# Kernel tuning notes

Measured on AMD Instinct MI355X. Metric: run time of the kernel, lower is better.

Reference implementation:

```python
import jax, jax.numpy as jnp
import numpy as np
import math

DIM = 1024
NUM_HEADS = 16
HEAD_DIM = DIM // NUM_HEADS
MAX_SEQ_LEN = 2048


def setup_inputs() -> dict:
    key = jax.random.key(0)
    ks = jax.random.split(key, 10)
    B, S = 4, 2048
    std = 1.0 / math.sqrt(DIM)
    inp = {
        "x": jax.random.normal(ks[0], (B, S, DIM), dtype=jnp.float32),
        "key_padding_mask": jnp.zeros((B, S), dtype=jnp.bool_),
        "q_w": jax.random.uniform(ks[1], (DIM, DIM), minval=-std, maxval=std),
        "q_b": jax.random.uniform(ks[2], (DIM,), minval=-std, maxval=std),
        "k_w": jax.random.uniform(ks[3], (DIM, DIM), minval=-std, maxval=std),
        "k_b": jax.random.uniform(ks[4], (DIM,), minval=-std, maxval=std),
        "v_w": jax.random.uniform(ks[5], (DIM, DIM), minval=-std, maxval=std),
        "v_b": jax.random.uniform(ks[6], (DIM,), minval=-std, maxval=std),
        "o_w": jax.random.uniform(ks[7], (DIM, DIM), minval=-std, maxval=std),
        "o_b": jax.random.uniform(ks[8], (DIM,), minval=-std, maxval=std),
    }
    return inp


def _rope_tables(seq_len):
    # freqs over half the head dim, per the RotaryPositionalEmbedding module
    half = HEAD_DIM // 2
    freqs = 1.0 / (10000.0 ** (jnp.arange(0, HEAD_DIM, 2, dtype=jnp.float32) / HEAD_DIM))
    pos = jnp.arange(seq_len, dtype=jnp.float32)
    ang = jnp.outer(pos, freqs)  # [S, half]
    return jnp.cos(ang)[:, :half], jnp.sin(ang)[:, :half]


def _apply_rope(t, cos, sin):
    # t: [B, H, S, D]; rotate first/second halves (non-interleaved variant)
    half = HEAD_DIM // 2
    left, right = t[..., :half], t[..., half:]
    return jnp.concatenate([left * cos - right * sin,
                            left * sin + right * cos], axis=-1)


def reference(x, key_padding_mask, q_w, q_b, k_w, k_b, v_w, v_b, o_w, o_b):
    B, S, _ = x.shape
    scale = HEAD_DIM ** -0.5

    def proj(w, b):
        y = jnp.einsum('bsd,ed->bse', x, w) + b  # torch Linear: x @ W^T + b
        return y.reshape(B, S, NUM_HEADS, HEAD_DIM).transpose(0, 2, 1, 3)

    q = proj(q_w, q_b)  # [B, H, S, D]
    k = proj(k_w, k_b)
    v = proj(v_w, v_b)

    cos, sin = _rope_tables(S)  # [S, half], broadcast over B,H
    q = _apply_rope(q, cos, sin)
    k = _apply_rope(k, cos, sin)

    scores = jnp.einsum('bhqd,bhkd->bhqk', q, k) * scale
    scores = jnp.where(key_padding_mask[:, None, None, :], -1e9, scores)
    weights = jax.nn.softmax(scores, axis=-1)  # dropout p=0.0 -> identity
    out = jnp.einsum('bhqk,bhkd->bhqd', weights, v)
    out = out.transpose(0, 2, 1, 3).reshape(B, S, DIM)
    return jnp.einsum('bsd,ed->bse', out, o_w) + o_b
```

## Files before the change

### kernel.cpp

```cpp
#include <hip/hip_runtime.h>
#include <stdint.h>

#define SEQ   2048
#define BATCH 4
#define NH    16
#define HD    64
#define DIMN  1024
#define MROWS (BATCH*SEQ)

typedef __attribute__((ext_vector_type(8)))  short          bf16x8;
typedef __attribute__((ext_vector_type(8)))  unsigned short ushort8;
typedef __attribute__((ext_vector_type(4)))  float          f32x4;
typedef __attribute__((ext_vector_type(16))) float          f32x16;

static __device__ __forceinline__ unsigned short f2bf(float f) {
    unsigned int u = __builtin_bit_cast(unsigned int, f);
    u += 0x7fffu + ((u >> 16) & 1u);
    return (unsigned short)(u >> 16);
}
static __device__ __forceinline__ unsigned int pack2bf(float lo, float hi) {
    unsigned int a = __builtin_bit_cast(unsigned int, lo) + 0x8000u;
    unsigned int b = __builtin_bit_cast(unsigned int, hi) + 0x8000u;
    return __builtin_amdgcn_perm(b, a, 0x07060302u);
}
static __device__ __forceinline__ unsigned int pack2bf_trunc(float lo, float hi) {
    return __builtin_amdgcn_perm(__builtin_bit_cast(unsigned int, hi),
                                 __builtin_bit_cast(unsigned int, lo), 0x07060302u);
}

__global__ __launch_bounds__(256) void prologue_kernel(
        const float* __restrict__ x,
        const float* __restrict__ qw, const float* __restrict__ kw,
        const float* __restrict__ vw, const float* __restrict__ ow,
        unsigned short* __restrict__ xb,
        unsigned short* __restrict__ wq, unsigned short* __restrict__ wk,
        unsigned short* __restrict__ wv, unsigned short* __restrict__ wo,
        float* __restrict__ cosT, float* __restrict__ sinT,
        const unsigned char* __restrict__ mask, unsigned long long* __restrict__ m64) {
    const int bx = blockIdx.x, tid = threadIdx.x;
    if (bx < 4096 + 2048) {
        const float* s; unsigned short* d; int i;
        if (bx < 4096) { s = x; d = xb; i = bx * 2048 + tid * 8; }
        else {
            int wb = bx - 4096;
            int wsel = wb >> 9;
            s = wsel == 0 ? qw : (wsel == 1 ? kw : (wsel == 2 ? vw : ow));
            d = wsel == 0 ? wq : (wsel == 1 ? wk : (wsel == 2 ? wv : wo));
            i = (wb & 511) * 2048 + tid * 8;
        }
        float4 a = *(const float4*)(s + i);
        float4 b = *(const float4*)(s + i + 4);
        ushort8 o;
        o[0]=f2bf(a.x); o[1]=f2bf(a.y); o[2]=f2bf(a.z); o[3]=f2bf(a.w);
        o[4]=f2bf(b.x); o[5]=f2bf(b.y); o[6]=f2bf(b.z); o[7]=f2bf(b.w);
        *(ushort8*)(d + i) = o;
    } else if (bx < 6400) {
        int idx = (bx - 6144) * 256 + tid;
        int s = idx >> 5, j = idx & 31;
        float t = (float)(2 * j) / 64.0f;
        float freq = 1.0f / powf(10000.0f, t);
        float ang  = (float)s * freq;
        cosT[idx] = cosf(ang);
        sinT[idx] = sinf(ang);
    } else {
        if (tid < 128) {
            int b = tid >> 5, kt = tid & 31;
            const unsigned char* p = mask + b * SEQ + kt * 64;
            unsigned long long v = 0;
            for (int j = 0; j < 64; j++) v |= (unsigned long long)(p[j] != 0) << j;
            m64[tid] = v;
        }
    }
}

__global__ __launch_bounds__(256) void gemm_qkvt(const unsigned short* __restrict__ X,
        const unsigned short* __restrict__ Wq, const unsigned short* __restrict__ Wk,
        const unsigned short* __restrict__ Wv,
        const float* __restrict__ bq, const float* __restrict__ bk, const float* __restrict__ bv,
        unsigned short* __restrict__ Qo, unsigned short* __restrict__ Ko, unsigned short* __restrict__ Vto,
        const float* __restrict__ cosT, const float* __restrict__ sinT) {
    __shared__ __align__(16) unsigned short As0[128 * 32];
    __shared__ __align__(16) unsigned short Bs0[128 * 32];
    __shared__ __align__(16) unsigned short As1[128 * 32];
    __shared__ __align__(16) unsigned short Bs1[128 * 32];
    const int which = blockIdx.x >> 3;
    const int tid  = threadIdx.x;
    const int wid  = tid >> 6, lane = tid & 63;
    const int quad = lane >> 4, l15 = lane & 15;
    const int wm   = wid >> 1,  wn  = wid & 1;

    const unsigned short *Ag, *Bg;
    int m0, n0;
    if (which < 2) {
        m0 = blockIdx.y * 128;
        n0 = (blockIdx.x & 7) * 128;
        Ag = X;  Bg = which == 0 ? Wq : Wk;
    } else {
        m0 = (blockIdx.x & 7) * 128;
        n0 = blockIdx.y * 128;
        Ag = Wv; Bg = X;
    }

    f32x4 acc[4][4];
#pragma unroll
    for (int i = 0; i < 4; i++)
#pragma unroll
        for (int j = 0; j < 4; j++) acc[i][j] = (f32x4)0.0f;

    const int rb = wid * 32 + (lane >> 2);
    const int cb = (((lane & 3) ^ ((lane >> 3) & 3)) * 8);
    const int rq = (quad ^ ((l15 >> 1) & 3)) * 8;

#define GSTAGE(BA, BB, KK) do {                                                             \
    _Pragma("unroll")                                                                       \
    for (int i_ = 0; i_ < 2; i_++) {                                                        \
        const unsigned short* ga_ = Ag + (size_t)(m0 + rb + i_ * 16) * DIMN + (KK) + cb;    \
        __builtin_amdgcn_global_load_lds((const __attribute__((address_space(1))) void*)ga_,\
            (__attribute__((address_space(3))) void*)&BA[(wid * 32 + i_ * 16) * 32], 16, 0, 0);\
        const unsigned short* gb_ = Bg + (size_t)(n0 + rb + i_ * 16) * DIMN + (KK) + cb;    \
        __builtin_amdgcn_global_load_lds((const __attribute__((address_space(1))) void*)gb_,\
            (__attribute__((address_space(3))) void*)&BB[(wid * 32 + i_ * 16) * 32], 16, 0, 0);\
    } } while (0)

#define GCOMP(BA, BB) do {                                                                  \
    bf16x8 af_[4], bf_[4];                                                                  \
    _Pragma("unroll")                                                                       \
    for (int f_ = 0; f_ < 4; f_++) af_[f_] = *(const bf16x8*)&BA[(wm * 64 + f_ * 16 + l15) * 32 + rq]; \
    _Pragma("unroll")                                                                       \
    for (int f_ = 0; f_ < 4; f_++) bf_[f_] = *(const bf16x8*)&BB[(wn * 64 + f_ * 16 + l15) * 32 + rq]; \
    _Pragma("unroll")                                                                       \
    for (int fm_ = 0; fm_ < 4; fm_++)                                                       \
        _Pragma("unroll")                                                                   \
        for (int fn_ = 0; fn_ < 4; fn_++)                                                   \
            acc[fm_][fn_] = __builtin_amdgcn_mfma_f32_16x16x32_bf16(af_[fm_], bf_[fn_], acc[fm_][fn_], 0, 0, 0); \
    } while (0)

    GSTAGE(As0, Bs0, 0);
    for (int k0 = 0; k0 < DIMN; k0 += 64) {
        __syncthreads();
        GSTAGE(As1, Bs1, k0 + 32);
        GCOMP(As0, Bs0);
        __syncthreads();
        if (k0 + 64 < DIMN) GSTAGE(As0, Bs0, k0 + 64);
        GCOMP(As1, Bs1);
    }

    if (which < 2) {
        const float* bias   = which == 0 ? bq : bk;
        unsigned short* Out = which == 0 ? Qo : Ko;
        const float scale = which == 0 ? 0.18033688011112042f : 1.0f;
        float bv4[4];
#pragma unroll
        for (int fn = 0; fn < 4; fn++) bv4[fn] = bias[n0 + wn * 64 + fn * 16 + l15];
        const int h = (n0 >> 6) + wn;
#pragma unroll
        for (int fm = 0; fm < 4; fm++)
#pragma unroll
            for (int r = 0; r < 4; r++) {
                int mrow = m0 + wm * 64 + fm * 16 + quad * 4 + r;
                int b = mrow >> 11, s = mrow & (SEQ - 1);
                unsigned short* orow = Out + ((size_t)(b * NH + h) * SEQ + s) * HD;
                float v0 = (acc[fm][0][r] + bv4[0]) * scale;
                float v1 = (acc[fm][1][r] + bv4[1]) * scale;
                float v2 = (acc[fm][2][r] + bv4[2]) * scale;
                float v3 = (acc[fm][3][r] + bv4[3]) * scale;
                int d0 = l15, d1 = 16 + l15;
                float c0 = cosT[s * 32 + d0], s0 = sinT[s * 32 + d0];
                float c1 = cosT[s * 32 + d1], s1 = sinT[s * 32 + d1];
                orow[d0]      = f2bf(v0 * c0 - v2 * s0);
                orow[d0 + 32] = f2bf(v0 * s0 + v2 * c0);
                orow[d1]      = f2bf(v1 * c1 - v3 * s1);
                orow[d1 + 32] = f2bf(v1 * s1 + v3 * c1);
            }
    } else {
        float4 bb[4];
#pragma unroll
        for (int fm = 0; fm < 4; fm++)
            bb[fm] = *(const float4*)&bv[m0 + wm * 64 + fm * 16 + quad * 4];
        const int b     = n0 >> 11;
        const int sbase = (n0 & (SEQ - 1)) + wn * 64 + l15;
#pragma unroll
        for (int fm = 0; fm < 4; fm++)
#pragma unroll
            for (int r = 0; r < 4; r++) {
                int e = m0 + wm * 64 + fm * 16 + quad * 4 + r;
                float bval = r == 0 ? bb[fm].x : (r == 1 ? bb[fm].y : (r == 2 ? bb[fm].z : bb[fm].w));
                unsigned short* row = Vto + ((size_t)(b * NH + (e >> 6)) * HD + (e & 63)) * SEQ + sbase;
#pragma unroll
                for (int fn = 0; fn < 4; fn++)
                    row[fn * 16] = f2bf(acc[fm][fn][r] + bval);
            }
    }
#undef GSTAGE
#undef GCOMP
}

__global__ __launch_bounds__(256) void gemm_bt(const unsigned short* __restrict__ A,
                                               const unsigned short* __restrict__ W,
                                               const float* __restrict__ bias,
                                               float* __restrict__ out) {
    __shared__ __align__(16) unsigned short As0[128 * 32];
    __shared__ __align__(16) unsigned short Bs0[128 * 32];
    __shared__ __align__(16) unsigned short As1[128 * 32];
    __shared__ __align__(16) unsigned short Bs1[128 * 32];
    const int tid  = threadIdx.x;
    const int wid  = tid >> 6, lane = tid & 63;
    const int quad = lane >> 4, l15 = lane & 15;
    const int wm   = wid >> 1,  wn  = wid & 1;
    const int m0   = blockIdx.y * 128, n0 = blockIdx.x * 128;

    f32x4 acc[4][4];
#pragma unroll
    for (int i = 0; i < 4; i++)
#pragma unroll
        for (int j = 0; j < 4; j++) acc[i][j] = (f32x4)0.0f;

    const int rb = wid * 32 + (lane >> 2);
    const int cb = (((lane & 3) ^ ((lane >> 3) & 3)) * 8);
    const int rq = (quad ^ ((l15 >> 1) & 3)) * 8;

#define GSTAGE(BA, BB, KK) do {                                                             \
    _Pragma("unroll")                                                                       \
    for (int i_ = 0; i_ < 2; i_++) {                                                        \
        const unsigned short* ga_ = A + (size_t)(m0 + rb + i_ * 16) * DIMN + (KK) + cb;     \
        __builtin_amdgcn_global_load_lds((const __attribute__((address_space(1))) void*)ga_,\
            (__attribute__((address_space(3))) void*)&BA[(wid * 32 + i_ * 16) * 32], 16, 0, 0);\
        const unsigned short* gb_ = W + (size_t)(n0 + rb + i_ * 16) * DIMN + (KK) + cb;     \
        __builtin_amdgcn_global_load_lds((const __attribute__((address_space(1))) void*)gb_,\
            (__attribute__((address_space(3))) void*)&BB[(wid * 32 + i_ * 16) * 32], 16, 0, 0);\
    } } while (0)

#define GCOMP(BA, BB) do {                                                                  \
    bf16x8 af_[4], bf_[4];                                                                  \
    _Pragma("unroll")                                                                       \
    for (int f_ = 0; f_ < 4; f_++) af_[f_] = *(const bf16x8*)&BA[(wm * 64 + f_ * 16 + l15) * 32 + rq]; \
    _Pragma("unroll")                                                                       \
    for (int f_ = 0; f_ < 4; f_++) bf_[f_] = *(const bf16x8*)&BB[(wn * 64 + f_ * 16 + l15) * 32 + rq]; \
    _Pragma("unroll")                                                                       \
    for (int fm_ = 0; fm_ < 4; fm_++)                                                       \
        _Pragma("unroll")                                                                   \
        for (int fn_ = 0; fn_ < 4; fn_++)                                                   \
            acc[fm_][fn_] = __builtin_amdgcn_mfma_f32_16x16x32_bf16(af_[fm_], bf_[fn_], acc[fm_][fn_], 0, 0, 0); \
    } while (0)

    GSTAGE(As0, Bs0, 0);
    for (int k0 = 0; k0 < DIMN; k0 += 64) {
        __syncthreads();
        GSTAGE(As1, Bs1, k0 + 32);
        GCOMP(As0, Bs0);
        __syncthreads();
        if (k0 + 64 < DIMN) GSTAGE(As0, Bs0, k0 + 64);
        GCOMP(As1, Bs1);
    }

    float bv4[4];
#pragma unroll
    for (int fn = 0; fn < 4; fn++) bv4[fn] = bias[n0 + wn * 64 + fn * 16 + l15];
#pragma unroll
    for (int fm = 0; fm < 4; fm++)
#pragma unroll
        for (int r = 0; r < 4; r++) {
            int mrow = m0 + wm * 64 + fm * 16 + quad * 4 + r;
            float* orow = out + (size_t)mrow * DIMN + n0 + wn * 64;
#pragma unroll
            for (int fn = 0; fn < 4; fn++) orow[fn * 16 + l15] = acc[fm][fn][r] + bv4[fn];
        }
#undef GSTAGE
#undef GCOMP
}

__global__ __launch_bounds__(256, 4) void attn_kernel(const unsigned short* __restrict__ Q,
                                                      const unsigned short* __restrict__ K,
                                                      const unsigned short* __restrict__ Vt,
                                                      const unsigned long long* __restrict__ M64,
                                                      unsigned short* __restrict__ Ob) {
    __shared__ __align__(16) unsigned short Kls[64 * 64];
    __shared__ __align__(16) unsigned short Vls[64 * 64];

    const int tid  = threadIdx.x;
    const int wid  = tid >> 6, lane = tid & 63;
    const int hi   = lane >> 5, l31 = lane & 31, l7 = lane & 7;
    const int bid = blockIdx.x;
    const int bh  = (bid & 7) * 8 + (bid >> 7);
    const int qt  = (bid >> 3) & 15;
    const int b = bh >> 4, h = bh & 15;
    const int q0 = qt * 128;

    bf16x8 qB[4];
    {
        const unsigned short* qrow = Q + ((size_t)bh * SEQ + q0 + wid * 32 + l31) * HD + hi * 8;
#pragma unroll
        for (int ks = 0; ks < 4; ks++)
            qB[ks] = __builtin_bit_cast(bf16x8, *(const uint4*)(qrow + ks * 16));
    }

    f32x16 Oa[2];
    Oa[0] = (f32x16)0.0f;
    Oa[1] = (f32x16)0.0f;
    float ls = 0.0f;

    const unsigned long long* Mrow = M64 + b * (SEQ / 64);

    const int srow = lane >> 3;
    const int sgr  = ((lane & 7) ^ ((lane >> 3) & 7)) * 8;
    const unsigned short* Kg = K  + (size_t)bh * SEQ * HD;
    const unsigned short* Vg = Vt + (size_t)bh * HD * SEQ;
    const unsigned short* Kb0 = Kg + (size_t)(wid * 16 + srow) * HD + sgr;
    const unsigned short* Vb0 = Vg + (size_t)(wid * 16 + srow) * SEQ + sgr;

    for (int kt = 0; kt < SEQ / 64; kt++) {
        const int k0 = kt * 64;
#pragma unroll
        for (int j = 0; j < 2; j++) {
            __builtin_amdgcn_global_load_lds(
                (const __attribute__((address_space(1))) void*)(Kb0 + (size_t)(k0 + j * 8) * HD),
                (__attribute__((address_space(3))) void*)&Kls[(wid * 16 + j * 8) * 64], 16, 0, 0);
            __builtin_amdgcn_global_load_lds(
                (const __attribute__((address_space(1))) void*)(Vb0 + (size_t)(j * 8) * SEQ + k0),
                (__attribute__((address_space(3))) void*)&Vls[(wid * 16 + j * 8) * 64], 16, 0, 0);
        }
        unsigned long long mb = Mrow[kt];
        __syncthreads();

#pragma unroll
        for (int h2 = 0; h2 < 2; h2++) {
            bf16x8 kA[4];
#pragma unroll
            for (int ks = 0; ks < 4; ks++)
                kA[ks] = *(const bf16x8*)&Kls[(h2 * 32 + l31) * 64 + (((ks << 1) + hi) ^ l7) * 8];

            f32x16 st = (f32x16)0.0f;
            __builtin_amdgcn_s_setprio(1);
#pragma unroll
            for (int ks = 0; ks < 4; ks++)
                st = __builtin_amdgcn_mfma_f32_32x32x16_bf16(kA[ks], qB[ks], st, 0, 0, 0);
            __builtin_amdgcn_s_setprio(0);

            unsigned int mh = (unsigned int)(mb >> (h2 * 32));
            if (mh) {
#pragma unroll
                for (int r = 0; r < 16; r++) {
                    int kk = (r & 3) + ((r >> 2) << 3) + (hi << 2);
                    if ((mh >> kk) & 1u) st[r] = -1e9f;
                }
            }

            float p[16];
#pragma unroll
            for (int r = 0; r < 16; r++) p[r] = __builtin_amdgcn_exp2f(st[r]);
            float s01 = (p[0] + p[1]) + (p[2] + p[3]);
            float s23 = (p[4] + p[5]) + (p[6] + p[7]);
            float s45 = (p[8] + p[9]) + (p[10] + p[11]);
            float s67 = (p[12] + p[13]) + (p[14] + p[15]);
            ls += (s01 + s23) + (s45 + s67);

            unsigned int w000 = pack2bf_trunc(p[0],  p[1]);
            unsigned int w001 = pack2bf_trunc(p[2],  p[3]);
            unsigned int w010 = pack2bf_trunc(p[4],  p[5]);
            unsigned int w011 = pack2bf_trunc(p[6],  p[7]);
            unsigned int w100 = pack2bf_trunc(p[8],  p[9]);
            unsigned int w101 = pack2bf_trunc(p[10], p[11]);
            unsigned int w110 = pack2bf_trunc(p[12], p[13]);
            unsigned int w111 = pack2bf_trunc(p[14], p[15]);

            bf16x8 pB[2];
#pragma unroll
            for (int ks = 0; ks < 2; ks++) {
                unsigned int own0 = ks == 0 ? (hi ? w010 : w000) : (hi ? w110 : w100);
                unsigned int own1 = ks == 0 ? (hi ? w011 : w001) : (hi ? w111 : w101);
                unsigned int oth0 = ks == 0 ? (hi ? w000 : w010) : (hi ? w100 : w110);
                unsigned int oth1 = ks == 0 ? (hi ? w001 : w011) : (hi ? w101 : w111);
                unsigned int r0 = (unsigned int)__shfl_xor((int)oth0, 32);
                unsigned int r1 = (unsigned int)__shfl_xor((int)oth1, 32);
                uint4 pw;
                pw.x = hi ? r0 : own0;
                pw.y = hi ? r1 : own1;
                pw.z = hi ? own0 : r0;
                pw.w = hi ? own1 : r1;
                pB[ks] = __builtin_bit_cast(bf16x8, pw);
            }

            __builtin_amdgcn_s_setprio(1);
#pragma unroll
            for (int dt = 0; dt < 2; dt++)
#pragma unroll
                for (int kv = 0; kv < 2; kv++) {
                    bf16x8 vA = *(const bf16x8*)&Vls[(dt * 32 + l31) * 64 +
                                    (((h2 << 2) + (kv << 1) + hi) ^ l7) * 8];
                    Oa[dt] = __builtin_amdgcn_mfma_f32_32x32x16_bf16(vA, pB[kv], Oa[dt], 0, 0, 0);
                }
            __builtin_amdgcn_s_setprio(0);
        }
        __syncthreads();
    }

    float lsum = ls + __shfl_xor(ls, 32);
    float linv = 1.0f / lsum;

    const int s = q0 + wid * 32 + l31;
    unsigned short* orow = Ob + ((size_t)b * SEQ + s) * DIMN + h * HD + hi * 4;
#pragma unroll
    for (int dt = 0; dt < 2; dt++)
#pragma unroll
        for (int rq = 0; rq < 4; rq++) {
            uint2 w;
            w.x = pack2bf(Oa[dt][rq * 4 + 0] * linv, Oa[dt][rq * 4 + 1] * linv);
            w.y = pack2bf(Oa[dt][rq * 4 + 2] * linv, Oa[dt][rq * 4 + 3] * linv);
            *(uint2*)&orow[dt * 32 + rq * 8] = w;
        }
}

extern "C" void kernel_launch(void* const* d_in, const int* in_sizes, int n_in,
                              void* d_out, int out_size, void* d_ws, size_t ws_size,
                              hipStream_t stream) {
    (void)in_sizes; (void)n_in; (void)out_size; (void)ws_size;
    const float* x  = (const float*)d_in[0];
    const unsigned char* mask = (const unsigned char*)d_in[1];
    const float* q_w = (const float*)d_in[2];
    const float* q_b = (const float*)d_in[3];
    const float* k_w = (const float*)d_in[4];
    const float* k_b = (const float*)d_in[5];
    const float* v_w = (const float*)d_in[6];
    const float* v_b = (const float*)d_in[7];
    const float* o_w = (const float*)d_in[8];
    const float* o_b = (const float*)d_in[9];
    float* out = (float*)d_out;

    char* w = (char*)d_ws;
    unsigned short* xb = (unsigned short*)w;
    unsigned short* wq = (unsigned short*)(w + (16u << 20));
    unsigned short* wk = wq + (1u << 20);
    unsigned short* wv = wk + (1u << 20);
    unsigned short* wo = wv + (1u << 20);
    float* cosT = (float*)(w + (24u << 20));
    float* sinT = cosT + SEQ * 32;
    unsigned long long* m64 = (unsigned long long*)(w + (24u << 20) + (1u << 19));
    unsigned short* Qb  = (unsigned short*)(w + (25u << 20));
    unsigned short* Kb  = Qb + (8u << 20);
    unsigned short* Vtb = Kb + (8u << 20);
    unsigned short* Ob  = xb;

    prologue_kernel<<<dim3(6401), 256, 0, stream>>>(x, q_w, k_w, v_w, o_w,
                                                    xb, wq, wk, wv, wo,
                                                    cosT, sinT, mask, m64);

    gemm_qkvt<<<dim3(24, 64), 256, 0, stream>>>(xb, wq, wk, wv, q_b, k_b, v_b,
                                                Qb, Kb, Vtb, cosT, sinT);

    attn_kernel<<<dim3(1024), 256, 0, stream>>>(Qb, Kb, Vtb, m64, Ob);

    gemm_bt<<<dim3(DIMN / 128, MROWS / 128), 256, 0, stream>>>(Ob, wo, o_b, out);
}
```

Baseline: 281.1 us.

## Split QKV GEMM into fused Q/K kernel sharing X tile and separate V kernel

The combined QKV GEMM is split in two. A new Q/K kernel loads each X tile once and computes both the Q and K products against it, which cuts X traffic and doubles the MFMA work per staged A tile. V is computed by its own transposed-output kernel. The cost is double the accumulator registers in the Q/K kernel, more LDS per block, an extra launch, and Q/K and V no longer sharing one grid.

```diff
diff --git a/kernel.cpp b/kernel.cpp
--- a/kernel.cpp
+++ b/kernel.cpp
@@ -73,33 +73,119 @@
     }
 }
 
-__global__ __launch_bounds__(256) void gemm_qkvt(const unsigned short* __restrict__ X,
+__global__ __launch_bounds__(256, 2) void gemm_qk(const unsigned short* __restrict__ X,
         const unsigned short* __restrict__ Wq, const unsigned short* __restrict__ Wk,
-        const unsigned short* __restrict__ Wv,
-        const float* __restrict__ bq, const float* __restrict__ bk, const float* __restrict__ bv,
-        unsigned short* __restrict__ Qo, unsigned short* __restrict__ Ko, unsigned short* __restrict__ Vto,
+        const float* __restrict__ bq, const float* __restrict__ bk,
+        unsigned short* __restrict__ Qo, unsigned short* __restrict__ Ko,
         const float* __restrict__ cosT, const float* __restrict__ sinT) {
+    __shared__ __align__(16) unsigned short As0[128 * 32];
+    __shared__ __align__(16) unsigned short Bq0[128 * 32];
+    __shared__ __align__(16) unsigned short Bk0[128 * 32];
+    __shared__ __align__(16) unsigned short As1[128 * 32];
+    __shared__ __align__(16) unsigned short Bq1[128 * 32];
+    __shared__ __align__(16) unsigned short Bk1[128 * 32];
+    const int tid  = threadIdx.x;
+    const int wid  = tid >> 6, lane = tid & 63;
+    const int quad = lane >> 4, l15 = lane & 15;
+    const int wm   = wid >> 1,  wn  = wid & 1;
+    const int m0   = blockIdx.y * 128;
+    const int n0   = blockIdx.x * 128;
+
+    f32x4 aq[4][4], ak[4][4];
+#pragma unroll
+    for (int i = 0; i < 4; i++)
+#pragma unroll
+        for (int j = 0; j < 4; j++) { aq[i][j] = (f32x4)0.0f; ak[i][j] = (f32x4)0.0f; }
+
+    const int rb = wid * 32 + (lane >> 2);
+    const int cb = (((lane & 3) ^ ((lane >> 3) & 3)) * 8);
+    const int rq = (quad ^ ((l15 >> 1) & 3)) * 8;
+
+#define QKSTAGE(AS, BQ, BK, KK) do {                                                        \
+    _Pragma("unroll")                                                                       \
+    for (int i_ = 0; i_ < 2; i_++) {                                                        \
+        const unsigned short* ga_ = X  + (size_t)(m0 + rb + i_ * 16) * DIMN + (KK) + cb;    \
+        __builtin_amdgcn_global_load_lds((const __attribute__((address_space(1))) void*)ga_,\
+            (__attribute__((address_space(3))) void*)&AS[(wid * 32 + i_ * 16) * 32], 16, 0, 0);\
+        const unsigned short* gq_ = Wq + (size_t)(n0 + rb + i_ * 16) * DIMN + (KK) + cb;    \
+        __builtin_amdgcn_global_load_lds((const __attribute__((address_space(1))) void*)gq_,\
+            (__attribute__((address_space(3))) void*)&BQ[(wid * 32 + i_ * 16) * 32], 16, 0, 0);\
+        const unsigned short* gk_ = Wk + (size_t)(n0 + rb + i_ * 16) * DIMN + (KK) + cb;    \
+        __builtin_amdgcn_global_load_lds((const __attribute__((address_space(1))) void*)gk_,\
+            (__attribute__((address_space(3))) void*)&BK[(wid * 32 + i_ * 16) * 32], 16, 0, 0);\
+    } } while (0)
+
+#define QKCOMP(AS, BQ, BK) do {                                                             \
+    bf16x8 af_[4], bqf_[4], bkf_[4];                                                        \
+    _Pragma("unroll")                                                                       \
+    for (int f_ = 0; f_ < 4; f_++) af_[f_]  = *(const bf16x8*)&AS[(wm * 64 + f_ * 16 + l15) * 32 + rq]; \
+    _Pragma("unroll")                                                                       \
+    for (int f_ = 0; f_ < 4; f_++) bqf_[f_] = *(const bf16x8*)&BQ[(wn * 64 + f_ * 16 + l15) * 32 + rq]; \
+    _Pragma("unroll")                                                                       \
+    for (int f_ = 0; f_ < 4; f_++) bkf_[f_] = *(const bf16x8*)&BK[(wn * 64 + f_ * 16 + l15) * 32 + rq]; \
+    _Pragma("unroll")                                                                       \
+    for (int fm_ = 0; fm_ < 4; fm_++)                                                       \
+        _Pragma("unroll")                                                                   \
+        for (int fn_ = 0; fn_ < 4; fn_++) {                                                 \
+            aq[fm_][fn_] = __builtin_amdgcn_mfma_f32_16x16x32_bf16(af_[fm_], bqf_[fn_], aq[fm_][fn_], 0, 0, 0); \
+            ak[fm_][fn_] = __builtin_amdgcn_mfma_f32_16x16x32_bf16(af_[fm_], bkf_[fn_], ak[fm_][fn_], 0, 0, 0); \
+        } } while (0)
+
+    QKSTAGE(As0, Bq0, Bk0, 0);
+    for (int k0 = 0; k0 < DIMN; k0 += 64) {
+        __syncthreads();
+        QKSTAGE(As1, Bq1, Bk1, k0 + 32);
+        QKCOMP(As0, Bq0, Bk0);
+        __syncthreads();
+        if (k0 + 64 < DIMN) QKSTAGE(As0, Bq0, Bk0, k0 + 64);
+        QKCOMP(As1, Bq1, Bk1);
+    }
+#undef QKSTAGE
+#undef QKCOMP
+
+    const int h = (n0 >> 6) + wn;
+#define QKEPI(ACC, BIAS, OUT, SCALE) do {                                                   \
+    float bv4_[4];                                                                          \
+    _Pragma("unroll")                                                                       \
+    for (int fn_ = 0; fn_ < 4; fn_++) bv4_[fn_] = BIAS[n0 + wn * 64 + fn_ * 16 + l15];      \
+    _Pragma("unroll")                                                                       \
+    for (int fm_ = 0; fm_ < 4; fm_++)                                                       \
+        _Pragma("unroll")                                                                   \
+        for (int r_ = 0; r_ < 4; r_++) {                                                    \
+            int mrow_ = m0 + wm * 64 + fm_ * 16 + quad * 4 + r_;                            \
+            int b_ = mrow_ >> 11, s_ = mrow_ & (SEQ - 1);                                   \
+            unsigned short* orow_ = OUT + ((size_t)(b_ * NH + h) * SEQ + s_) * HD;          \
+            float v0_ = (ACC[fm_][0][r_] + bv4_[0]) * (SCALE);                              \
+            float v1_ = (ACC[fm_][1][r_] + bv4_[1]) * (SCALE);                              \
+            float v2_ = (ACC[fm_][2][r_] + bv4_[2]) * (SCALE);                              \
+            float v3_ = (ACC[fm_][3][r_] + bv4_[3]) * (SCALE);                              \
+            int d0_ = l15, d1_ = 16 + l15;                                                  \
+            float c0_ = cosT[s_ * 32 + d0_], s0_ = sinT[s_ * 32 + d0_];                     \
+            float c1_ = cosT[s_ * 32 + d1_], s1_ = sinT[s_ * 32 + d1_];                     \
+            orow_[d0_]      = f2bf(v0_ * c0_ - v2_ * s0_);                                  \
+            orow_[d0_ + 32] = f2bf(v0_ * s0_ + v2_ * c0_);                                  \
+            orow_[d1_]      = f2bf(v1_ * c1_ - v3_ * s1_);                                  \
+            orow_[d1_ + 32] = f2bf(v1_ * s1_ + v3_ * c1_);                                  \
+        } } while (0)
+
+    QKEPI(aq, bq, Qo, 0.18033688011112042f);
+    QKEPI(ak, bk, Ko, 1.0f);
+#undef QKEPI
+}
+
+__global__ __launch_bounds__(256) void gemm_vt(const unsigned short* __restrict__ Wv,
+        const unsigned short* __restrict__ X, const float* __restrict__ bv,
+        unsigned short* __restrict__ Vto) {
     __shared__ __align__(16) unsigned short As0[128 * 32];
     __shared__ __align__(16) unsigned short Bs0[128 * 32];
     __shared__ __align__(16) unsigned short As1[128 * 32];
     __shared__ __align__(16) unsigned short Bs1[128 * 32];
-    const int which = blockIdx.x >> 3;
     const int tid  = threadIdx.x;
     const int wid  = tid >> 6, lane = tid & 63;
     const int quad = lane >> 4, l15 = lane & 15;
     const int wm   = wid >> 1,  wn  = wid & 1;
-
-    const unsigned short *Ag, *Bg;
-    int m0, n0;
-    if (which < 2) {
-        m0 = blockIdx.y * 128;
-        n0 = (blockIdx.x & 7) * 128;
-        Ag = X;  Bg = which == 0 ? Wq : Wk;
-    } else {
-        m0 = (blockIdx.x & 7) * 128;
-        n0 = blockIdx.y * 128;
-        Ag = Wv; Bg = X;
-    }
+    const int m0   = blockIdx.x * 128;
+    const int n0   = blockIdx.y * 128;
 
     f32x4 acc[4][4];
 #pragma unroll
@@ -114,10 +200,10 @@
 #define GSTAGE(BA, BB, KK) do {                                                             \
     _Pragma("unroll")                                                                       \
     for (int i_ = 0; i_ < 2; i_++) {                                                        \
-        const unsigned short* ga_ = Ag + (size_t)(m0 + rb + i_ * 16) * DIMN + (KK) + cb;    \
+        const unsigned short* ga_ = Wv + (size_t)(m0 + rb + i_ * 16) * DIMN + (KK) + cb;    \
         __builtin_amdgcn_global_load_lds((const __attribute__((address_space(1))) void*)ga_,\
             (__attribute__((address_space(3))) void*)&BA[(wid * 32 + i_ * 16) * 32], 16, 0, 0);\
-        const unsigned short* gb_ = Bg + (size_t)(n0 + rb + i_ * 16) * DIMN + (KK) + cb;    \
+        const unsigned short* gb_ = X + (size_t)(n0 + rb + i_ * 16) * DIMN + (KK) + cb;     \
         __builtin_amdgcn_global_load_lds((const __attribute__((address_space(1))) void*)gb_,\
             (__attribute__((address_space(3))) void*)&BB[(wid * 32 + i_ * 16) * 32], 16, 0, 0);\
     } } while (0)
@@ -145,52 +231,23 @@
         GCOMP(As1, Bs1);
     }
 
-    if (which < 2) {
-        const float* bias   = which == 0 ? bq : bk;
-        unsigned short* Out = which == 0 ? Qo : Ko;
-        const float scale = which == 0 ? 0.18033688011112042f : 1.0f;
-        float bv4[4];
-#pragma unroll
-        for (int fn = 0; fn < 4; fn++) bv4[fn] = bias[n0 + wn * 64 + fn * 16 + l15];
-        const int h = (n0 >> 6) + wn;
-#pragma unroll
-        for (int fm = 0; fm < 4; fm++)
-#pragma unroll
-            for (int r = 0; r < 4; r++) {
-                int mrow = m0 + wm * 64 + fm * 16 + quad * 4 + r;
-                int b = mrow >> 11, s = mrow & (SEQ - 1);
-                unsigned short* orow = Out + ((size_t)(b * NH + h) * SEQ + s) * HD;
-                float v0 = (acc[fm][0][r] + bv4[0]) * scale;
-                float v1 = (acc[fm][1][r] + bv4[1]) * scale;
-                float v2 = (acc[fm][2][r] + bv4[2]) * scale;
-                float v3 = (acc[fm][3][r] + bv4[3]) * scale;
-                int d0 = l15, d1 = 16 + l15;
-                float c0 = cosT[s * 32 + d0], s0 = sinT[s * 32 + d0];
-                float c1 = cosT[s * 32 + d1], s1 = sinT[s * 32 + d1];
-                orow[d0]      = f2bf(v0 * c0 - v2 * s0);
-                orow[d0 + 32] = f2bf(v0 * s0 + v2 * c0);
-                orow[d1]      = f2bf(v1 * c1 - v3 * s1);
-                orow[d1 + 32] = f2bf(v1 * s1 + v3 * c1);
-            }
-    } else {
-        float4 bb[4];
-#pragma unroll
-        for (int fm = 0; fm < 4; fm++)
-            bb[fm] = *(const float4*)&bv[m0 + wm * 64 + fm * 16 + quad * 4];
-        const int b     = n0 >> 11;
-        const int sbase = (n0 & (SEQ - 1)) + wn * 64 + l15;
-#pragma unroll
-        for (int fm = 0; fm < 4; fm++)
-#pragma unroll
-            for (int r = 0; r < 4; r++) {
-                int e = m0 + wm * 64 + fm * 16 + quad * 4 + r;
-                float bval = r == 0 ? bb[fm].x : (r == 1 ? bb[fm].y : (r == 2 ? bb[fm].z : bb[fm].w));
-                unsigned short* row = Vto + ((size_t)(b * NH + (e >> 6)) * HD + (e & 63)) * SEQ + sbase;
-#pragma unroll
-                for (int fn = 0; fn < 4; fn++)
-                    row[fn * 16] = f2bf(acc[fm][fn][r] + bval);
-            }
-    }
+    float4 bb[4];
+#pragma unroll
+    for (int fm = 0; fm < 4; fm++)
+        bb[fm] = *(const float4*)&bv[m0 + wm * 64 + fm * 16 + quad * 4];
+    const int b     = n0 >> 11;
+    const int sbase = (n0 & (SEQ - 1)) + wn * 64 + l15;
+#pragma unroll
+    for (int fm = 0; fm < 4; fm++)
+#pragma unroll
+        for (int r = 0; r < 4; r++) {
+            int e = m0 + wm * 64 + fm * 16 + quad * 4 + r;
+            float bval = r == 0 ? bb[fm].x : (r == 1 ? bb[fm].y : (r == 2 ? bb[fm].z : bb[fm].w));
+            unsigned short* row = Vto + ((size_t)(b * NH + (e >> 6)) * HD + (e & 63)) * SEQ + sbase;
+#pragma unroll
+            for (int fn = 0; fn < 4; fn++)
+                row[fn * 16] = f2bf(acc[fm][fn][r] + bval);
+        }
 #undef GSTAGE
 #undef GCOMP
 }
@@ -444,8 +501,8 @@
                                                     xb, wq, wk, wv, wo,
                                                     cosT, sinT, mask, m64);
 
-    gemm_qkvt<<<dim3(24, 64), 256, 0, stream>>>(xb, wq, wk, wv, q_b, k_b, v_b,
-                                                Qb, Kb, Vtb, cosT, sinT);
+    gemm_qk<<<dim3(8, 64), 256, 0, stream>>>(xb, wq, wk, q_b, k_b, Qb, Kb, cosT, sinT);
+    gemm_vt<<<dim3(8, 64), 256, 0, stream>>>(wv, xb, v_b, Vtb);
 
     attn_kernel<<<dim3(1024), 256, 0, stream>>>(Qb, Kb, Vtb, m64, Ob);
 
```

Result: no change. 286.4 us (+1.9%).

## Split attention along KV into two partial kernels plus a normalization pass

Applied to the files above, without the earlier changes.

Attention is split into two KV halves per query tile, giving twice as many blocks with higher occupancy bounds. Each half writes unnormalized fp32 outputs and row sums to workspace, and a separate kernel sums the halves, normalizes, and writes bf16. This is meant to raise parallelism and latency hiding, at the cost of large extra fp32 memory traffic and an additional launch. It falls back to the original kernel when the workspace is too small.

```diff
diff --git a/kernel.cpp b/kernel.cpp
--- a/kernel.cpp
+++ b/kernel.cpp
@@ -269,11 +269,12 @@
 #undef GCOMP
 }
 
-__global__ __launch_bounds__(256, 4) void attn_kernel(const unsigned short* __restrict__ Q,
-                                                      const unsigned short* __restrict__ K,
-                                                      const unsigned short* __restrict__ Vt,
-                                                      const unsigned long long* __restrict__ M64,
-                                                      unsigned short* __restrict__ Ob) {
+__global__ __launch_bounds__(256, 8) void attn_part(const unsigned short* __restrict__ Q,
+                                                    const unsigned short* __restrict__ K,
+                                                    const unsigned short* __restrict__ Vt,
+                                                    const unsigned long long* __restrict__ M64,
+                                                    float* __restrict__ Opart,
+                                                    float* __restrict__ Lpart) {
     __shared__ __align__(16) unsigned short Kls[64 * 64];
     __shared__ __align__(16) unsigned short Vls[64 * 64];
 
@@ -281,9 +282,10 @@
     const int wid  = tid >> 6, lane = tid & 63;
     const int hi   = lane >> 5, l31 = lane & 31, l7 = lane & 7;
     const int bid = blockIdx.x;
-    const int bh  = (bid & 7) * 8 + (bid >> 7);
-    const int qt  = (bid >> 3) & 15;
-    const int b = bh >> 4, h = bh & 15;
+    const int bh  = (bid & 7) * 8 + (bid >> 8);
+    const int mid = (bid >> 3) & 31;
+    const int qt  = mid >> 1, sh = mid & 1;
+    const int b = bh >> 4;
     const int q0 = qt * 128;
 
     bf16x8 qB[4];
@@ -308,7 +310,7 @@
     const unsigned short* Kb0 = Kg + (size_t)(wid * 16 + srow) * HD + sgr;
     const unsigned short* Vb0 = Vg + (size_t)(wid * 16 + srow) * SEQ + sgr;
 
-    for (int kt = 0; kt < SEQ / 64; kt++) {
+    for (int kt = sh * 16; kt < sh * 16 + 16; kt++) {
         const int k0 = kt * 64;
 #pragma unroll
         for (int j = 0; j < 2; j++) {
@@ -395,6 +397,183 @@
     }
 
     float lsum = ls + __shfl_xor(ls, 32);
+    const int ql = wid * 32 + l31;
+    const size_t part = (size_t)((bh * 16 + qt) * 2 + sh);
+    if (hi == 0) Lpart[part * 128 + ql] = lsum;
+
+    float* Op = Opart + part * (128 * 64) + (size_t)ql * 64;
+#pragma unroll
+    for (int dt = 0; dt < 2; dt++)
+#pragma unroll
+        for (int rg = 0; rg < 4; rg++) {
+            float4 v;
+            v.x = Oa[dt][rg * 4 + 0];
+            v.y = Oa[dt][rg * 4 + 1];
+            v.z = Oa[dt][rg * 4 + 2];
+            v.w = Oa[dt][rg * 4 + 3];
+            *(float4*)(Op + dt * 32 + rg * 8 + hi * 4) = v;
+        }
+}
+
+__global__ __launch_bounds__(256) void attn_norm(const float* __restrict__ Opart,
+                                                 const float* __restrict__ Lpart,
+                                                 unsigned short* __restrict__ Ob) {
+    const int bq = blockIdx.x;
+    const int bh = bq >> 4, qt = bq & 15;
+    const int b = bh >> 4, h = bh & 15;
+    const int tid = threadIdx.x;
+    const int q = tid >> 1, dh = (tid & 1) * 32;
+
+    const float l0 = Lpart[(size_t)(bq * 2 + 0) * 128 + q];
+    const float l1 = Lpart[(size_t)(bq * 2 + 1) * 128 + q];
+    const float linv = 1.0f / (l0 + l1);
+
+    const float* O0 = Opart + (size_t)(bq * 2 + 0) * (128 * 64) + (size_t)q * 64 + dh;
+    const float* O1 = O0 + 128 * 64;
+
+    const int s = qt * 128 + q;
+    unsigned short* orow = Ob + ((size_t)b * SEQ + s) * DIMN + h * HD + dh;
+#pragma unroll
+    for (int g = 0; g < 4; g++) {
+        float4 a0 = *(const float4*)(O0 + g * 8);
+        float4 a1 = *(const float4*)(O0 + g * 8 + 4);
+        float4 c0 = *(const float4*)(O1 + g * 8);
+        float4 c1 = *(const float4*)(O1 + g * 8 + 4);
+        uint4 st;
+        st.x = pack2bf((a0.x + c0.x) * linv, (a0.y + c0.y) * linv);
+        st.y = pack2bf((a0.z + c0.z) * linv, (a0.w + c0.w) * linv);
+        st.z = pack2bf((a1.x + c1.x) * linv, (a1.y + c1.y) * linv);
+        st.w = pack2bf((a1.z + c1.z) * linv, (a1.w + c1.w) * linv);
+        *(uint4*)(orow + g * 8) = st;
+    }
+}
+
+__global__ __launch_bounds__(256, 4) void attn_kernel(const unsigned short* __restrict__ Q,
+                                                      const unsigned short* __restrict__ K,
+                                                      const unsigned short* __restrict__ Vt,
+                                                      const unsigned long long* __restrict__ M64,
+                                                      unsigned short* __restrict__ Ob) {
+    __shared__ __align__(16) unsigned short Kls[64 * 64];
+    __shared__ __align__(16) unsigned short Vls[64 * 64];
+
+    const int tid  = threadIdx.x;
+    const int wid  = tid >> 6, lane = tid & 63;
+    const int hi   = lane >> 5, l31 = lane & 31, l7 = lane & 7;
+    const int bid = blockIdx.x;
+    const int bh  = (bid & 7) * 8 + (bid >> 7);
+    const int qt  = (bid >> 3) & 15;
+    const int b = bh >> 4, h = bh & 15;
+    const int q0 = qt * 128;
+
+    bf16x8 qB[4];
+    {
+        const unsigned short* qrow = Q + ((size_t)bh * SEQ + q0 + wid * 32 + l31) * HD + hi * 8;
+#pragma unroll
+        for (int ks = 0; ks < 4; ks++)
+            qB[ks] = __builtin_bit_cast(bf16x8, *(const uint4*)(qrow + ks * 16));
+    }
+
+    f32x16 Oa[2];
+    Oa[0] = (f32x16)0.0f;
+    Oa[1] = (f32x16)0.0f;
+    float ls = 0.0f;
+
+    const unsigned long long* Mrow = M64 + b * (SEQ / 64);
+
+    const int srow = lane >> 3;
+    const int sgr  = ((lane & 7) ^ ((lane >> 3) & 7)) * 8;
+    const unsigned short* Kg = K  + (size_t)bh * SEQ * HD;
+    const unsigned short* Vg = Vt + (size_t)bh * HD * SEQ;
+    const unsigned short* Kb0 = Kg + (size_t)(wid * 16 + srow) * HD + sgr;
+    const unsigned short* Vb0 = Vg + (size_t)(wid * 16 + srow) * SEQ + sgr;
+
+    for (int kt = 0; kt < SEQ / 64; kt++) {
+        const int k0 = kt * 64;
+#pragma unroll
+        for (int j = 0; j < 2; j++) {
+            __builtin_amdgcn_global_load_lds(
+                (const __attribute__((address_space(1))) void*)(Kb0 + (size_t)(k0 + j * 8) * HD),
+                (__attribute__((address_space(3))) void*)&Kls[(wid * 16 + j * 8) * 64], 16, 0, 0);
+            __builtin_amdgcn_global_load_lds(
+                (const __attribute__((address_space(1))) void*)(Vb0 + (size_t)(j * 8) * SEQ + k0),
+                (__attribute__((address_space(3))) void*)&Vls[(wid * 16 + j * 8) * 64], 16, 0, 0);
+        }
+        unsigned long long mb = Mrow[kt];
+        __syncthreads();
+
+#pragma unroll
+        for (int h2 = 0; h2 < 2; h2++) {
+            bf16x8 kA[4];
+#pragma unroll
+            for (int ks = 0; ks < 4; ks++)
+                kA[ks] = *(const bf16x8*)&Kls[(h2 * 32 + l31) * 64 + (((ks << 1) + hi) ^ l7) * 8];
+
+            f32x16 st = (f32x16)0.0f;
+            __builtin_amdgcn_s_setprio(1);
+#pragma unroll
+            for (int ks = 0; ks < 4; ks++)
+                st = __builtin_amdgcn_mfma_f32_32x32x16_bf16(kA[ks], qB[ks], st, 0, 0, 0);
+            __builtin_amdgcn_s_setprio(0);
+
+            unsigned int mh = (unsigned int)(mb >> (h2 * 32));
+            if (mh) {
+#pragma unroll
+                for (int r = 0; r < 16; r++) {
+                    int kk = (r & 3) + ((r >> 2) << 3) + (hi << 2);
+                    if ((mh >> kk) & 1u) st[r] = -1e9f;
+                }
+            }
+
+            float p[16];
+#pragma unroll
+            for (int r = 0; r < 16; r++) p[r] = __builtin_amdgcn_exp2f(st[r]);
+            float s01 = (p[0] + p[1]) + (p[2] + p[3]);
+            float s23 = (p[4] + p[5]) + (p[6] + p[7]);
+            float s45 = (p[8] + p[9]) + (p[10] + p[11]);
+            float s67 = (p[12] + p[13]) + (p[14] + p[15]);
+            ls += (s01 + s23) + (s45 + s67);
+
+            unsigned int w000 = pack2bf_trunc(p[0],  p[1]);
+            unsigned int w001 = pack2bf_trunc(p[2],  p[3]);
+            unsigned int w010 = pack2bf_trunc(p[4],  p[5]);
+            unsigned int w011 = pack2bf_trunc(p[6],  p[7]);
+            unsigned int w100 = pack2bf_trunc(p[8],  p[9]);
+            unsigned int w101 = pack2bf_trunc(p[10], p[11]);
+            unsigned int w110 = pack2bf_trunc(p[12], p[13]);
+            unsigned int w111 = pack2bf_trunc(p[14], p[15]);
+
+            bf16x8 pB[2];
+#pragma unroll
+            for (int ks = 0; ks < 2; ks++) {
+                unsigned int own0 = ks == 0 ? (hi ? w010 : w000) : (hi ? w110 : w100);
+                unsigned int own1 = ks == 0 ? (hi ? w011 : w001) : (hi ? w111 : w101);
+                unsigned int oth0 = ks == 0 ? (hi ? w000 : w010) : (hi ? w100 : w110);
+                unsigned int oth1 = ks == 0 ? (hi ? w001 : w011) : (hi ? w101 : w111);
+                unsigned int r0 = (unsigned int)__shfl_xor((int)oth0, 32);
+                unsigned int r1 = (unsigned int)__shfl_xor((int)oth1, 32);
+                uint4 pw;
+                pw.x = hi ? r0 : own0;
+                pw.y = hi ? r1 : own1;
+                pw.z = hi ? own0 : r0;
+                pw.w = hi ? own1 : r1;
+                pB[ks] = __builtin_bit_cast(bf16x8, pw);
+            }
+
+            __builtin_amdgcn_s_setprio(1);
+#pragma unroll
+            for (int dt = 0; dt < 2; dt++)
+#pragma unroll
+                for (int kv = 0; kv < 2; kv++) {
+                    bf16x8 vA = *(const bf16x8*)&Vls[(dt * 32 + l31) * 64 +
+                                    (((h2 << 2) + (kv << 1) + hi) ^ l7) * 8];
+                    Oa[dt] = __builtin_amdgcn_mfma_f32_32x32x16_bf16(vA, pB[kv], Oa[dt], 0, 0, 0);
+                }
+            __builtin_amdgcn_s_setprio(0);
+        }
+        __syncthreads();
+    }
+
+    float lsum = ls + __shfl_xor(ls, 32);
     float linv = 1.0f / lsum;
 
     const int s = q0 + wid * 32 + l31;
@@ -413,7 +592,7 @@
 extern "C" void kernel_launch(void* const* d_in, const int* in_sizes, int n_in,
                               void* d_out, int out_size, void* d_ws, size_t ws_size,
                               hipStream_t stream) {
-    (void)in_sizes; (void)n_in; (void)out_size; (void)ws_size;
+    (void)in_sizes; (void)n_in; (void)out_size;
     const float* x  = (const float*)d_in[0];
     const unsigned char* mask = (const unsigned char*)d_in[1];
     const float* q_w = (const float*)d_in[2];
@@ -439,6 +618,8 @@
     unsigned short* Kb  = Qb + (8u << 20);
     unsigned short* Vtb = Kb + (8u << 20);
     unsigned short* Ob  = xb;
+    float* Opart = (float*)(w + (73u << 20));
+    float* Lpart = (float*)(w + (137u << 20));
 
     prologue_kernel<<<dim3(6401), 256, 0, stream>>>(x, q_w, k_w, v_w, o_w,
                                                     xb, wq, wk, wv, wo,
@@ -447,7 +628,12 @@
     gemm_qkvt<<<dim3(24, 64), 256, 0, stream>>>(xb, wq, wk, wv, q_b, k_b, v_b,
                                                 Qb, Kb, Vtb, cosT, sinT);
 
-    attn_kernel<<<dim3(1024), 256, 0, stream>>>(Qb, Kb, Vtb, m64, Ob);
+    if (ws_size >= (138ull << 20)) {
+        attn_part<<<dim3(2048), 256, 0, stream>>>(Qb, Kb, Vtb, m64, Opart, Lpart);
+        attn_norm<<<dim3(1024), 256, 0, stream>>>(Opart, Lpart, Ob);
+    } else {
+        attn_kernel<<<dim3(1024), 256, 0, stream>>>(Qb, Kb, Vtb, m64, Ob);
+    }
 
     gemm_bt<<<dim3(DIMN / 128, MROWS / 128), 256, 0, stream>>>(Ob, wo, o_b, out);
 }
```

Result: slower. 715.1 us (+154.4%).
